# Performance work log

Hardware: AMD Instinct MI355X
Metric: run time of the kernel (lower is better)

Reference implementation:

```python
import jax, jax.numpy as jnp
import numpy as np

# hyperparams matching init_kwargs
T_LEN = 1024
T_LATENCY = 7
TB = T_LATENCY + 1          # t_len_block
N_OUT = 1024
BATCH = 32
FS_SCALE = 10.0             # FastSigmoid default scale


@jax.custom_vjp
def fast_sigmoid(x):
    # forward: Heaviside; backward: fast-sigmoid surrogate
    return (x > 0).astype(x.dtype)

def _fs_fwd(x):
    return (x > 0).astype(x.dtype), x

def _fs_bwd(x, g):
    return (g / (FS_SCALE * jnp.abs(x) + 1.0) ** 2,)

fast_sigmoid.defvjp(_fs_fwd, _fs_bwd)


def setup_inputs() -> dict:
    key = jax.random.key(0)
    k1, k2, k3, k4 = jax.random.split(key, 4)
    x = jax.random.normal(k1, (T_LEN, BATCH, N_OUT), dtype=jnp.float32) * 0.6
    # raw params; forward applies the clamp/abs 'properties' of the module
    beta_raw = jax.random.uniform(k2, (N_OUT,), minval=0.7, maxval=0.99, dtype=jnp.float32)
    p_raw = jax.random.uniform(k3, (N_OUT,), minval=0.5, maxval=0.95, dtype=jnp.float32)
    b_raw = jax.random.uniform(k4, (N_OUT,), minval=0.2, maxval=1.0, dtype=jnp.float32)
    return {"x": x, "beta_raw": beta_raw, "p_raw": p_raw, "b_raw": b_raw}


def reference(x, beta_raw, p_raw, b_raw):
    T, B, N = x.shape
    tb = TB
    n_blocks = T // tb  # t_pad == 0 by construction
    dt = x.dtype

    # clamped properties
    beta = jnp.clip(beta_raw, 0.001, 0.999)          # [N]
    p = jnp.clip(jnp.abs(p_raw), 0.0, 0.999)         # [N]
    bb = jnp.clip(jnp.abs(b_raw), 0.001, 1.0)        # [N]

    t_idx = jnp.arange(tb)
    expo = t_idx[:, None] - t_idx[None, :]            # [tb,tb], t - s
    lower = expo >= 0
    # causal decay kernel: beta^(t-s) for s<=t  (grouped conv1d equivalent)
    beta_pow = jnp.where(lower[:, :, None],
                         beta[None, None, :] ** jnp.maximum(expo, 0)[:, :, None].astype(dt),
                         jnp.zeros((), dt))           # [tb,tb,N]
    # phi kernel: weight (t-s+1) for s<=t  (conv2d equivalent)
    phi = jnp.where(lower, (expo + 1).astype(dt), jnp.zeros((), dt))  # [tb,tb]
    p_exp = jnp.arange(1, tb + 1, dtype=dt)           # [tb]
    p_pow = p[None, :] ** p_exp[:, None]              # [tb,N]
    inv_p = 1.0 / p                                   # [N]

    def body(carry, x_slice):
        spikes, z, int_mem, a_kernel = carry          # [tb,B,N],[tb,B,N],[B,N],[tb,B,N]
        sg = jax.lax.stop_gradient(spikes)            # detach_spike_grad=True
        maskf = (jnp.max(sg, axis=0) > 0).astype(dt)  # [B,N] any spike in prev block
        # refractory masking of input
        xs = jnp.where(z < maskf[None], jnp.zeros((), dt), x_slice)
        v_init = int_mem * (1.0 - maskf)
        # adaptation update
        a_at_spike = jnp.sum(a_kernel * sg, axis=0) + inv_p          # [B,N]
        decay_steps = jnp.sum(z > 1, axis=0).astype(dt)              # [B,N]
        new_a = a_at_spike * jnp.power(p[None, :], decay_steps)
        a = a_kernel[-1] * (1.0 - maskf) + new_a * maskf             # [B,N]
        a_k = p_pow[:, None, :] * a[None]                             # [tb,B,N]
        v_th = 1.0 + bb[None, None, :] * a_k                          # [tb,B,N]
        # --- Block forward ---
        cur = xs.at[0].add(beta[None, :] * v_init)
        membrane = jnp.einsum('tsn,sbn->tbn', beta_pow, cur)          # causal decayed sum
        faulty = fast_sigmoid(membrane - v_th)                        # [tb,B,N] 0/1
        z_new = jnp.einsum('ts,sbn->tbn', phi, faulty)
        # g(): keep only entries exactly 1, straight-through grad
        spikes_new = z_new - jax.lax.stop_gradient(
            jnp.where(z_new == 1.0, jnp.zeros((), dt), z_new))
        return (spikes_new, z_new, membrane[-1], a_k), spikes_new

    z0 = jnp.zeros((tb, B, N), dt)
    carry0 = (z0, z0, jnp.zeros((B, N), dt), z0)
    xb = x.reshape(n_blocks, tb, B, N)
    _, out = jax.lax.scan(body, carry0, xb)
    return out.reshape(T, B, N)
```

## Files before the change

kernel.cpp:

```cpp
#include <hip/hip_runtime.h>


constexpr int T_LEN = 1024;
constexpr int TB    = 8;
constexpr int NBLK  = T_LEN / TB;
constexpr int BATCH = 32;
constexpr int NOUT  = 1024;
constexpr int BN    = BATCH * NOUT;
constexpr int PF    = 8;

typedef float f4 __attribute__((ext_vector_type(4)));

__global__ __launch_bounds__(64, 1)
void snn_blocks_kernel(const float* __restrict__ x,
                       const float* __restrict__ beta_raw,
                       const float* __restrict__ p_raw,
                       const float* __restrict__ b_raw,
                       float* __restrict__ out)
{
    __shared__ float inbuf[TB][64];
    __shared__ float sbuf[TB][64];

    const int lane = threadIdx.x;
    const int wg0  = blockIdx.x * 64;
    const int gid  = wg0 + lane;
    const int n    = gid & (NOUT - 1);

    const int rowoff = lane >> 4;
    const int coloff = wg0 + (lane & 15) * 4;

    double beta = (double)beta_raw[n];
    beta = beta < 0.001 ? 0.001 : (beta > 0.999 ? 0.999 : beta);
    double p = fabs((double)p_raw[n]);
    p = p > 0.999 ? 0.999 : p;
    double bb = fabs((double)b_raw[n]);
    bb = bb < 0.001 ? 0.001 : (bb > 1.0 ? 1.0 : bb);
    const double inv_p = 1.0 / p;

    double ppow[9];
    ppow[0] = 1.0;
#pragma unroll
    for (int i = 1; i <= 8; ++i) ppow[i] = ppow[i - 1] * p;

    double bbp[8];
#pragma unroll
    for (int t = 0; t < 8; ++t) bbp[t] = bb * ppow[t + 1];

    double m = 0.0;
    double a = 0.0;
    int    maskf = 0;
    int    decay = 0;
    double ssum  = 0.0;
    int    zzero = 0xFF;

    f4 fr[PF][2];

    const float* xbase = x + (ptrdiff_t)rowoff * BN + coloff;

#pragma unroll
    for (int k = 0; k < PF; ++k) {
        fr[k][0] = *(const f4*)(xbase + (ptrdiff_t)(k * TB) * BN);
        fr[k][1] = *(const f4*)(xbase + (ptrdiff_t)(k * TB + 4) * BN);
    }

    auto body = [&](int blk, f4 v0, f4 v1) {
        *(f4*)&inbuf[rowoff][(lane & 15) * 4]     = v0;
        *(f4*)&inbuf[rowoff + 4][(lane & 15) * 4] = v1;
        float cur[8];
#pragma unroll
        for (int t = 0; t < 8; ++t) cur[t] = inbuf[t][lane];

        const double a_at = a * ssum + inv_p;
        double pd = 1.0;
        pd *= (decay & 1) ? p       : 1.0;
        pd *= (decay & 2) ? ppow[2] : 1.0;
        pd *= (decay & 4) ? ppow[4] : 1.0;
        pd *= (decay & 8) ? ppow[8] : 1.0;
        const double new_a = a_at * pd;

        if (maskf) { a = new_a;     m = 0.0; }
        else       { a = ppow[8] * a;        }

        int nmaskf = 0, ndecay = 0, nzzero = 0;
        double nssum = 0.0;
        int c = 0, zc = 0;
#pragma unroll
        for (int t = 0; t < 8; ++t) {
            double xv = (double)cur[t];
            if (maskf && ((zzero >> t) & 1)) xv = 0.0;
            m = beta * m + xv;
            const double vth = 1.0 + bbp[t] * a;
            const int f = (m - vth > 0.0) ? 1 : 0;
            c  += f;
            zc += c;
            nmaskf |= (zc == 1);
            ndecay += (zc > 1) ? 1 : 0;
            nssum  += (zc == 1) ? ppow[t + 1] : 0.0;
            nzzero |= (zc == 0) ? (1 << t) : 0;
            sbuf[t][lane] = (zc == 1) ? 1.0f : 0.0f;
        }
        maskf = nmaskf; decay = ndecay; ssum = nssum; zzero = nzzero;

        const float* sflat = &sbuf[0][0];
        f4 s0 = *(const f4*)(sflat + lane * 4);
        f4 s1 = *(const f4*)(sflat + 256 + lane * 4);
        __builtin_nontemporal_store(
            s0, (f4*)(out + (ptrdiff_t)(blk * TB + rowoff) * BN + coloff));
        __builtin_nontemporal_store(
            s1, (f4*)(out + (ptrdiff_t)(blk * TB + 4 + rowoff) * BN + coloff));
    };

#pragma unroll 1
    for (int r = 0; r < NBLK / PF; ++r) {
#pragma unroll
        for (int i = 0; i < PF; ++i) {
            const int blk = r * PF + i;
            body(blk, fr[i][0], fr[i][1]);
            const int pfb = blk + PF;
            if (pfb < NBLK) {
                fr[i][0] = *(const f4*)(xbase + (ptrdiff_t)(pfb * TB) * BN);
                fr[i][1] = *(const f4*)(xbase + (ptrdiff_t)(pfb * TB + 4) * BN);
            }
            __builtin_amdgcn_sched_barrier(0);
        }
    }
}

extern "C" void kernel_launch(void* const* d_in, const int* in_sizes, int n_in,
                              void* d_out, int out_size, void* d_ws, size_t ws_size,
                              hipStream_t stream) {
    const float* x        = (const float*)d_in[0];
    const float* beta_raw = (const float*)d_in[1];
    const float* p_raw    = (const float*)d_in[2];
    const float* b_raw    = (const float*)d_in[3];
    float* out            = (float*)d_out;

    dim3 grid(BN / 64);
    dim3 block(64);
    snn_blocks_kernel<<<grid, block, 0, stream>>>(x, beta_raw, p_raw, b_raw, out);
}
```

Measured before the change: 243.8 us.

## Simplify spike recurrence to first-spike index and drop LDS transpose

Rewrites the per-block recurrence around the first spike index. The spike output becomes a one-hot at the first crossing, and the decay-step count and surrogate sum are derived algebraically from that index instead of being tracked with cumulative counters. The LDS transpose buffers are removed: each lane now loads and stores scalar floats directly along time, and the prefetch depth is halved. This cuts ALU work and LDS traffic, at the risk of less efficient scalar memory accesses. It also relies on the recurrence simplification being exact for all inputs.

```diff
diff --git a/kernel.cpp b/kernel.cpp
--- a/kernel.cpp
+++ b/kernel.cpp
@@ -7,9 +7,7 @@
 constexpr int BATCH = 32;
 constexpr int NOUT  = 1024;
 constexpr int BN    = BATCH * NOUT;
-constexpr int PF    = 8;
-
-typedef float f4 __attribute__((ext_vector_type(4)));
+constexpr int PF    = 4;
 
 __global__ __launch_bounds__(64, 1)
 void snn_blocks_kernel(const float* __restrict__ x,
@@ -18,16 +16,9 @@
                        const float* __restrict__ b_raw,
                        float* __restrict__ out)
 {
-    __shared__ float inbuf[TB][64];
-    __shared__ float sbuf[TB][64];
-
     const int lane = threadIdx.x;
-    const int wg0  = blockIdx.x * 64;
-    const int gid  = wg0 + lane;
+    const int gid  = blockIdx.x * 64 + lane;
     const int n    = gid & (NOUT - 1);
-
-    const int rowoff = lane >> 4;
-    const int coloff = wg0 + (lane & 15) * 4;
 
     double beta = (double)beta_raw[n];
     beta = beta < 0.001 ? 0.001 : (beta > 0.999 ? 0.999 : beta);
@@ -46,80 +37,69 @@
 #pragma unroll
     for (int t = 0; t < 8; ++t) bbp[t] = bb * ppow[t + 1];
 
+    const double pp2 = ppow[2], pp4 = ppow[4], pp8 = ppow[8];
+
     double m = 0.0;
     double a = 0.0;
-    int    maskf = 0;
-    int    decay = 0;
-    double ssum  = 0.0;
-    int    zzero = 0xFF;
+    int maskf  = 0;
+    int firstp = 0;
 
-    f4 fr[PF][2];
-
-    const float* xbase = x + (ptrdiff_t)rowoff * BN + coloff;
+    float fr[PF][8];
+    const float* xb = x + gid;
+    float* ob       = out + gid;
 
 #pragma unroll
-    for (int k = 0; k < PF; ++k) {
-        fr[k][0] = *(const f4*)(xbase + (ptrdiff_t)(k * TB) * BN);
-        fr[k][1] = *(const f4*)(xbase + (ptrdiff_t)(k * TB + 4) * BN);
-    }
-
-    auto body = [&](int blk, f4 v0, f4 v1) {
-        *(f4*)&inbuf[rowoff][(lane & 15) * 4]     = v0;
-        *(f4*)&inbuf[rowoff + 4][(lane & 15) * 4] = v1;
-        float cur[8];
+    for (int k = 0; k < PF; ++k)
 #pragma unroll
-        for (int t = 0; t < 8; ++t) cur[t] = inbuf[t][lane];
-
-        const double a_at = a * ssum + inv_p;
-        double pd = 1.0;
-        pd *= (decay & 1) ? p       : 1.0;
-        pd *= (decay & 2) ? ppow[2] : 1.0;
-        pd *= (decay & 4) ? ppow[4] : 1.0;
-        pd *= (decay & 8) ? ppow[8] : 1.0;
-        const double new_a = a_at * pd;
-
-        if (maskf) { a = new_a;     m = 0.0; }
-        else       { a = ppow[8] * a;        }
-
-        int nmaskf = 0, ndecay = 0, nzzero = 0;
-        double nssum = 0.0;
-        int c = 0, zc = 0;
-#pragma unroll
-        for (int t = 0; t < 8; ++t) {
-            double xv = (double)cur[t];
-            if (maskf && ((zzero >> t) & 1)) xv = 0.0;
-            m = beta * m + xv;
-            const double vth = 1.0 + bbp[t] * a;
-            const int f = (m - vth > 0.0) ? 1 : 0;
-            c  += f;
-            zc += c;
-            nmaskf |= (zc == 1);
-            ndecay += (zc > 1) ? 1 : 0;
-            nssum  += (zc == 1) ? ppow[t + 1] : 0.0;
-            nzzero |= (zc == 0) ? (1 << t) : 0;
-            sbuf[t][lane] = (zc == 1) ? 1.0f : 0.0f;
-        }
-        maskf = nmaskf; decay = ndecay; ssum = nssum; zzero = nzzero;
-
-        const float* sflat = &sbuf[0][0];
-        f4 s0 = *(const f4*)(sflat + lane * 4);
-        f4 s1 = *(const f4*)(sflat + 256 + lane * 4);
-        __builtin_nontemporal_store(
-            s0, (f4*)(out + (ptrdiff_t)(blk * TB + rowoff) * BN + coloff));
-        __builtin_nontemporal_store(
-            s1, (f4*)(out + (ptrdiff_t)(blk * TB + 4 + rowoff) * BN + coloff));
-    };
+        for (int t = 0; t < 8; ++t)
+            fr[k][t] = xb[(ptrdiff_t)(k * TB + t) * BN];
 
 #pragma unroll 1
     for (int r = 0; r < NBLK / PF; ++r) {
 #pragma unroll
         for (int i = 0; i < PF; ++i) {
             const int blk = r * PF + i;
-            body(blk, fr[i][0], fr[i][1]);
+
+            double pf1 = p;
+            pf1 *= (firstp & 1) ? p   : 1.0;
+            pf1 *= (firstp & 2) ? pp2 : 1.0;
+            pf1 *= (firstp & 4) ? pp4 : 1.0;
+            const int dsteps = firstp ^ 7;
+            double pd = (dsteps & 1) ? p : 1.0;
+            pd *= (dsteps & 2) ? pp2 : 1.0;
+            pd *= (dsteps & 4) ? pp4 : 1.0;
+            const double new_a = (a * pf1 + inv_p) * pd;
+            double vinit;
+            if (maskf) { a = new_a;   vinit = 0.0; }
+            else       { a = pp8 * a; vinit = m;   }
+
+            const int zmask = maskf ? ((1 << firstp) - 1) : 0;
+
+            int fbits = 0;
+            double mm = vinit;
+#pragma unroll
+            for (int t = 0; t < 8; ++t) {
+                const float xf = ((zmask >> t) & 1) ? 0.0f : fr[i][t];
+                mm = beta * mm + (double)xf;
+                const double vth = 1.0 + bbp[t] * a;
+                fbits |= (mm - vth > 0.0) ? (1 << t) : 0;
+            }
+            m = mm;
+            maskf  = (fbits != 0);
+            firstp = fbits ? __builtin_ctz(fbits) : 0;
+
+#pragma unroll
+            for (int t = 0; t < 8; ++t) {
+                const float sv = (maskf && t == firstp) ? 1.0f : 0.0f;
+                __builtin_nontemporal_store(
+                    sv, ob + (ptrdiff_t)(blk * TB + t) * BN);
+            }
+
             const int pfb = blk + PF;
             if (pfb < NBLK) {
-                fr[i][0] = *(const f4*)(xbase + (ptrdiff_t)(pfb * TB) * BN);
-                fr[i][1] = *(const f4*)(xbase + (ptrdiff_t)(pfb * TB + 4) * BN);
+#pragma unroll
+                for (int t = 0; t < 8; ++t)
+                    fr[i][t] = xb[(ptrdiff_t)(pfb * TB + t) * BN];
             }
             __builtin_amdgcn_sched_barrier(0);
         }
```

Result: slower. 255.4 us (+4.7%).
